# Optimization experiments

Hardware: AMD Instinct MI355X
Metric: run time of the kernel (lower is better)

## Reference

```python
import jax, jax.numpy as jnp
import numpy as np

NPOINT = 1024
RADIUS = 0.15
NSAMPLE = 32
BN_EPS = 1e-5


def farthest_point_sample(xyz, npoint):
    # xyz: [B, N, 3] -> idx [B, npoint]
    B, N, _ = xyz.shape

    def step(carry, _):
        dmin, far = carry
        cent = jnp.take_along_axis(xyz, far[:, None, None], axis=1)  # [B,1,3]
        d = jnp.sum((xyz - cent) ** 2, axis=-1)                      # [B,N]
        dmin = jnp.minimum(dmin, d)
        nxt = jnp.argmax(dmin, axis=-1).astype(jnp.int32)
        return (dmin, nxt), far

    init = (jnp.full((B, N), 1e10, xyz.dtype), jnp.zeros((B,), jnp.int32))
    _, idx = jax.lax.scan(step, init, None, length=npoint)
    return idx.T  # [B, npoint]


def ball_query(radius, nsample, xyz, new_xyz):
    # xyz: [B,N,3], new_xyz: [B,S,3] -> idx [B,S,nsample]
    B, S, _ = new_xyz.shape
    N = xyz.shape[1]
    sqr = jnp.sum((new_xyz[:, :, None, :] - xyz[:, None, :, :]) ** 2, axis=-1)  # [B,S,N]
    ar = jnp.broadcast_to(jnp.arange(N, dtype=jnp.int32), (B, S, N))
    gidx = jnp.where(sqr > radius * radius, N, ar)
    gidx = jnp.sort(gidx, axis=-1)[:, :, :nsample]
    first = gidx[:, :, :1]
    return jnp.where(gidx == N, first, gidx)


def setup_inputs() -> dict:
    key = jax.random.key(0)
    ks = jax.random.split(key, 8)
    B, N, Cin, Cmlp, Cout = 8, 4096, 64, 128, 256
    xyz = jax.random.uniform(ks[0], (B, N, 3), dtype=jnp.float32)
    t = jax.random.normal(ks[1], (B, 128), dtype=jnp.float32)
    points = jax.random.normal(ks[2], (B, N, Cin), dtype=jnp.float32)
    W1 = jax.random.normal(ks[3], (Cin, Cmlp), dtype=jnp.float32) / np.sqrt(Cin)
    b1 = jnp.zeros((Cmlp,), jnp.float32)
    Wc = jax.random.normal(ks[4], (Cmlp, Cout), dtype=jnp.float32) / np.sqrt(Cmlp)
    bc = jnp.zeros((Cout,), jnp.float32)
    gamma = jnp.ones((Cout,), jnp.float32)
    beta = jnp.zeros((Cout,), jnp.float32)
    return {"xyz": xyz, "t": t, "points": points, "W1": W1, "b1": b1,
            "Wc": Wc, "bc": bc, "gamma": gamma, "beta": beta}


def reference(xyz, t, points, W1, b1, Wc, bc, gamma, beta):
    # t (time embedding) is unused in the visible (truncated) forward body.
    B, N, _ = xyz.shape
    # 1) farthest point sampling -> centers
    fps_idx = farthest_point_sample(xyz, NPOINT)                     # [B,S]
    new_xyz = jnp.take_along_axis(xyz, fps_idx[:, :, None], axis=1)  # [B,S,3]
    # 2) radius ball-query grouping
    gidx = ball_query(RADIUS, NSAMPLE, xyz, new_xyz)                 # [B,S,ns]
    # 3) pointwise MLP on features, then group (gather)
    feats = points @ W1 + b1                                          # [B,N,Cmlp]
    grouped = jax.vmap(lambda f, i: f[i])(feats, gidx)                # [B,S,ns,Cmlp]
    # 4) GroupConv: 1x1 conv + BatchNorm(train stats) + ReLU
    h = jnp.einsum('bsnc,co->bsno', grouped, Wc) + bc                 # [B,S,ns,Cout]
    mean = jnp.mean(h, axis=(0, 1, 2))
    var = jnp.var(h, axis=(0, 1, 2))
    h = jax.nn.relu((h - mean) / jnp.sqrt(var + BN_EPS) * gamma + beta)
    # 5) max-pool over neighborhood
    new_points = jnp.max(h, axis=2)                                   # [B,S,Cout]
    return new_points
```

## Files before the change

kernel.cpp:

```cpp
#include <hip/hip_runtime.h>
#include <stdint.h>

#define BN 8
#define NPT 4096
#define NS 1024
#define KS 32
#define CIN 64
#define CMID 128
#define COUT 256
#define NGRP (BN*NS)
#define NBINS 512

typedef short bf16x8 __attribute__((ext_vector_type(8)));
typedef float f32x4 __attribute__((ext_vector_type(4)));
typedef unsigned long long u64;

__device__ __forceinline__ float bf2f(unsigned short u){
  union { unsigned int i; float f; } v; v.i = ((unsigned int)u) << 16; return v.f;
}
__device__ __forceinline__ unsigned short f2bf(float f){
  union { float f; unsigned int i; } v; v.f = f;
  unsigned int r = (v.i + 0x7fffu + ((v.i >> 16) & 1u)) >> 16;
  return (unsigned short)r;
}
__device__ __forceinline__ uint32_t pack2(float a, float b){
  return (uint32_t)f2bf(a) | ((uint32_t)f2bf(b) << 16);
}
__device__ __forceinline__ float ldf(const void* p, size_t i, bool isbf){
  return isbf ? bf2f(((const unsigned short*)p)[i]) : ((const float*)p)[i];
}
__device__ __forceinline__ bool detect_bf(const void* gamma){
  return ((const unsigned int*)gamma)[0] == 0x3F803F80u;
}
template<int CTRL>
__device__ __forceinline__ u64 dpp_rot_u64(u64 x){
  int lo = (int)(unsigned int)(x & 0xFFFFFFFFull);
  int hi = (int)(unsigned int)(x >> 32);
  int nlo = __builtin_amdgcn_update_dpp(0, lo, CTRL, 0xF, 0xF, true);
  int nhi = __builtin_amdgcn_update_dpp(0, hi, CTRL, 0xF, 0xF, true);
  return ((u64)(unsigned int)nhi << 32) | (unsigned int)nlo;
}
__device__ __forceinline__ u64 u64max(u64 a, u64 b){ return a > b ? a : b; }

__device__ __forceinline__ unsigned mcode(float x, float y, float z){
  int ix = (int)(x*16.f); ix = ix<0?0:(ix>15?15:ix);
  int iy = (int)(y*16.f); iy = iy<0?0:(iy>15?15:iy);
  int iz = (int)(z*8.f);  iz = iz<0?0:(iz>7?7:iz);
  return ((unsigned)(iy&1))      | ((unsigned)(ix&1)<<1) | ((unsigned)(iz&1)<<2)
       | ((unsigned)(iy&2)<<2)   | ((unsigned)(ix&2)<<3) | ((unsigned)(iz&2)<<4)
       | ((unsigned)(iy&4)<<4)   | ((unsigned)(ix&4)<<5) | ((unsigned)(iz&4)<<6)
       | ((unsigned)(iy&8)<<6)   | ((unsigned)(ix&8)<<7);
}

__global__ __launch_bounds__(512, 4)
void k_front(const void* __restrict__ xyz,
             const void* __restrict__ points,
             const void* __restrict__ W1,
             const void* __restrict__ Wc,
             const void* __restrict__ gamma,
             float* __restrict__ newxyz,
             unsigned short* __restrict__ featsb,
             unsigned short* __restrict__ wct,
             float* __restrict__ ps, float* __restrict__ pq, int bigws)
{
  int tid = threadIdx.x;
  int bid = blockIdx.x;
  bool isbf = detect_bf(gamma);
  __shared__ __align__(16) char smem[65536];
  __shared__ unsigned tsum[512];
  __shared__ u64 wk[2][8];

  if (bid < 8){
    float* ssx = (float*)smem;
    float* ssy = ssx + NPT;
    float* ssz = ssy + NPT;
    unsigned short* snl = (unsigned short*)(ssz + NPT);
    unsigned* hist = (unsigned*)(smem + 57344);
    size_t xb = (size_t)bid*NPT*3;
    int base = tid*8;
    for (int i=tid; i<2048; i+=512) hist[i]=0;
    __syncthreads();
    unsigned codes[8];
    #pragma unroll
    for (int k=0;k<8;k++){
      size_t p = xb + (size_t)(base+k)*3;
      unsigned c = mcode(ldf(xyz,p,isbf), ldf(xyz,p+1,isbf), ldf(xyz,p+2,isbf));
      codes[k]=c;
      atomicAdd(&hist[c],1u);
    }
    __syncthreads();
    unsigned l0=hist[tid*4],l1=hist[tid*4+1],l2=hist[tid*4+2],l3=hist[tid*4+3];
    unsigned s = l0+l1+l2+l3;
    tsum[tid]=s; __syncthreads();
    for (int off=1; off<512; off<<=1){
      unsigned v = (tid>=off)? tsum[tid-off]:0u; __syncthreads();
      tsum[tid]+=v; __syncthreads();
    }
    unsigned ex = tsum[tid]-s;
    hist[tid*4]=ex; hist[tid*4+1]=ex+l0; hist[tid*4+2]=ex+l0+l1; hist[tid*4+3]=ex+l0+l1+l2;
    __syncthreads();
    #pragma unroll
    for (int k=0;k<8;k++){
      size_t p = xb + (size_t)(base+k)*3;
      float x=ldf(xyz,p,isbf), y=ldf(xyz,p+1,isbf), z=ldf(xyz,p+2,isbf);
      unsigned pos = atomicAdd(&hist[codes[k]],1u);
      ssx[pos]=x; ssy[pos]=y; ssz[pos]=z; snl[pos]=(unsigned short)(4095-(base+k));
    }
    __syncthreads();
    float qx0,qx1,qx2,qx3,qx4,qx5,qx6,qx7;
    float qy0,qy1,qy2,qy3,qy4,qy5,qy6,qy7;
    float qz0,qz1,qz2,qz3,qz4,qz5,qz6,qz7;
    float dd0,dd1,dd2,dd3,dd4,dd5,dd6,dd7;
    unsigned lk0,lk1,lk2,lk3,lk4,lk5,lk6,lk7;
#define LOADS(k) { int p=base+k; qx##k=ssx[p]; qy##k=ssy[p]; qz##k=ssz[p]; dd##k=1e10f; \
  lk##k = ((unsigned)snl[p]<<12) | (unsigned)p; }
    LOADS(0) LOADS(1) LOADS(2) LOADS(3) LOADS(4) LOADS(5) LOADS(6) LOADS(7)
#undef LOADS
    float bxl = fminf(fminf(fminf(qx0,qx1),fminf(qx2,qx3)),fminf(fminf(qx4,qx5),fminf(qx6,qx7)));
    float bxh = fmaxf(fmaxf(fmaxf(qx0,qx1),fmaxf(qx2,qx3)),fmaxf(fmaxf(qx4,qx5),fmaxf(qx6,qx7)));
    float byl = fminf(fminf(fminf(qy0,qy1),fminf(qy2,qy3)),fminf(fminf(qy4,qy5),fminf(qy6,qy7)));
    float byh = fmaxf(fmaxf(fmaxf(qy0,qy1),fmaxf(qy2,qy3)),fmaxf(fmaxf(qy4,qy5),fmaxf(qy6,qy7)));
    float bzl = fminf(fminf(fminf(qz0,qz1),fminf(qz2,qz3)),fminf(fminf(qz4,qz5),fminf(qz6,qz7)));
    float bzh = fmaxf(fmaxf(fmaxf(qz0,qz1),fmaxf(qz2,qz3)),fmaxf(fmaxf(qz4,qz5),fmaxf(qz6,qz7)));
    #pragma unroll
    for (int off=1; off<64; off<<=1){
      bxl = fminf(bxl, __shfl_xor(bxl,off,64)); bxh = fmaxf(bxh, __shfl_xor(bxh,off,64));
      byl = fminf(byl, __shfl_xor(byl,off,64)); byh = fmaxf(byh, __shfl_xor(byh,off,64));
      bzl = fminf(bzl, __shfl_xor(bzl,off,64)); bzh = fmaxf(bzh, __shfl_xor(bzh,off,64));
    }
    float cx=ldf(xyz,xb,isbf), cy=ldf(xyz,xb+1,isbf), cz=ldf(xyz,xb+2,isbf);
    if (tid==0){ float* o = newxyz + (size_t)bid*NS*3; o[0]=cx; o[1]=cy; o[2]=cz; }
    int lane = tid & 63, wv = tid >> 6;
    u64 ckey = ((u64)__float_as_uint(1e10f) << 32);
    for (int it=1; it<NS; ++it){
      int par = it & 1;
      float ex2 = fmaxf(fmaxf(__fsub_rn(bxl,cx), __fsub_rn(cx,bxh)), 0.f);
      float ey2 = fmaxf(fmaxf(__fsub_rn(byl,cy), __fsub_rn(cy,byh)), 0.f);
      float ez2 = fmaxf(fmaxf(__fsub_rn(bzl,cz), __fsub_rn(cz,bzh)), 0.f);
      float lb2 = ex2*ex2 + ey2*ey2 + ez2*ez2;
      float wtmax = __uint_as_float((unsigned)(ckey >> 32));
      bool act = !(lb2*0.999f >= wtmax);
      if (__builtin_amdgcn_readfirstlane((int)act)){
#define FPS_STEP(k) { float dx=__fsub_rn(qx##k,cx), dy=__fsub_rn(qy##k,cy), dz=__fsub_rn(qz##k,cz); \
  float d=__fadd_rn(__fadd_rn(__fmul_rn(dx,dx),__fmul_rn(dy,dy)),__fmul_rn(dz,dz)); \
  dd##k=fminf(dd##k,d); }
        FPS_STEP(0) FPS_STEP(1) FPS_STEP(2) FPS_STEP(3)
        FPS_STEP(4) FPS_STEP(5) FPS_STEP(6) FPS_STEP(7)
#undef FPS_STEP
#define KEYK(k) ( ((u64)__float_as_uint(dd##k) << 32) | lk##k )
        u64 e0=u64max(KEYK(0),KEYK(1)), e2=u64max(KEYK(2),KEYK(3));
        u64 e4=u64max(KEYK(4),KEYK(5)), e6=u64max(KEYK(6),KEYK(7));
#undef KEYK
        e0=u64max(e0,e2); e4=u64max(e4,e6);
        u64 key=u64max(e0,e4);
        key = u64max(key, dpp_rot_u64<0x121>(key));
        key = u64max(key, dpp_rot_u64<0x122>(key));
        key = u64max(key, dpp_rot_u64<0x124>(key));
        key = u64max(key, dpp_rot_u64<0x128>(key));
        key = u64max(key, __shfl_xor(key, 16, 64));
        key = u64max(key, __shfl_xor(key, 32, 64));
        ckey = key;
      }
      if (lane == 0) wk[par][wv] = ckey;
      __syncthreads();
      const u64* w8 = wk[par];
      u64 k0 = u64max(u64max(u64max(w8[0],w8[1]), u64max(w8[2],w8[3])),
                      u64max(u64max(w8[4],w8[5]), u64max(w8[6],w8[7])));
      unsigned spos = (unsigned)(k0 & 0xFFFu);
      cx = ssx[spos]; cy = ssy[spos]; cz = ssz[spos];
      if (tid==0){ float* o = newxyz + ((size_t)bid*NS + it)*3; o[0]=cx; o[1]=cy; o[2]=cz; }
    }
  } else if (bid == 8){
    for (int i=tid; i<CMID*COUT; i+=512){
      int k = i >> 8, n = i & 255;
      unsigned short w = isbf ? ((const unsigned short*)Wc)[i] : f2bf(((const float*)Wc)[i]);
      wct[(size_t)n*CMID + k] = w;
    }
    if (!bigws){
      for (int i=tid; i<COUT*NBINS; i+=512){ ps[i]=0.f; pq[i]=0.f; }
    }
  } else {
    float* w1s = (float*)smem;
    float* pts = (float*)(smem + 32768);
    int rb = bid - 9;
    int r0g = rb*64;
    for (int i=tid; i<CIN*CMID; i+=512) w1s[i] = ldf(W1, i, isbf);
    for (int i=tid; i<64*CIN; i+=512)   pts[i] = ldf(points, (size_t)r0g*CIN + i, isbf);
    __syncthreads();
    int o0 = (tid & 15) * 8, r0 = (tid >> 4) * 2;
    float acc0[8]={0,0,0,0,0,0,0,0}, acc1[8]={0,0,0,0,0,0,0,0};
    for (int c=0;c<CIN;c++){
      float a0 = pts[r0*CIN + c], a1 = pts[(r0+1)*CIN + c];
      const float* wr = &w1s[c*CMID + o0];
      #pragma unroll
      for (int j=0;j<8;j++){ acc0[j] = fmaf(a0, wr[j], acc0[j]); acc1[j] = fmaf(a1, wr[j], acc1[j]); }
    }
    unsigned short* f0 = featsb + ((size_t)(r0g + r0))*CMID + o0;
    uint4 u;
    u.x=pack2(acc0[0],acc0[1]); u.y=pack2(acc0[2],acc0[3]); u.z=pack2(acc0[4],acc0[5]); u.w=pack2(acc0[6],acc0[7]);
    *(uint4*)f0 = u;
    u.x=pack2(acc1[0],acc1[1]); u.y=pack2(acc1[2],acc1[3]); u.z=pack2(acc1[4],acc1[5]); u.w=pack2(acc1[6],acc1[7]);
    *(uint4*)(f0 + CMID) = u;
  }
}

__global__ __launch_bounds__(256)
void k_ballq(const void* __restrict__ xyz,
             const void* __restrict__ gamma,
             const float* __restrict__ newxyz,
             int* __restrict__ gidx)
{
  __shared__ float sp[NPT*3];
  __shared__ int slots[4][KS];
  int tid = threadIdx.x;
  bool isbf = detect_bf(gamma);
  int cb = blockIdx.x * 64;
  int b = cb >> 10;
  size_t xb = (size_t)b*NPT*3;
  for (int i=tid; i<NPT*3; i+=256) sp[i] = ldf(xyz, xb + i, isbf);
  __syncthreads();
  int lane = tid & 63, wv = tid >> 6;
  const float rr = (float)(0.15*0.15);
  for (int j=0; j<16; ++j){
    int cid = cb + wv*16 + j;
    const float* cc = newxyz + (size_t)cid*3;
    float cx=cc[0], cy=cc[1], cz=cc[2];
    int cnt = 0;
    for (int ch=0; ch<64; ++ch){
      int p = ch*64 + lane;
      float dx=__fsub_rn(sp[p*3],cx), dy=__fsub_rn(sp[p*3+1],cy), dz=__fsub_rn(sp[p*3+2],cz);
      float d=__fadd_rn(__fadd_rn(__fmul_rn(dx,dx),__fmul_rn(dy,dy)),__fmul_rn(dz,dz));
      bool in = !(d > rr);
      u64 mk = __ballot(in);
      int pos = cnt + __popcll(mk & ((1ull<<lane) - 1ull));
      if (in && pos < KS) slots[wv][pos] = p;
      cnt += __popcll(mk);
      if (cnt >= KS) break;
    }
    int total = cnt < KS ? cnt : KS;
    if (lane < KS){
      int v = (lane < total) ? slots[wv][lane] : slots[wv][0];
      gidx[(size_t)cid*KS + lane] = v;
    }
  }
}

__global__ __launch_bounds__(256)
void k_group(const unsigned short* __restrict__ featsb,
             const unsigned short* __restrict__ wct,
             const int* __restrict__ gidx,
             float* __restrict__ ps, float* __restrict__ pq,
             float* __restrict__ hM, int bigws)
{
  int tid = threadIdx.x;
  int bs0 = blockIdx.x * 2;
  __shared__ unsigned short g[2][32][136];
  __shared__ int gi[2][KS];
  if (tid < 2*KS) gi[tid>>5][tid&31] = gidx[(size_t)bs0*KS + tid];
  __syncthreads();
  {
    int r = tid >> 3, sg = tid & 7;
    size_t fb = (size_t)(bs0>>10)*NPT;
    #pragma unroll
    for (int gg=0; gg<2; gg++){
      const unsigned short* src = featsb + (fb + gi[gg][r])*CMID + sg*16;
      uint4 v0 = *(const uint4*)src;
      uint4 v1 = *(const uint4*)(src + 8);
      *(uint4*)(&g[gg][r][sg*16])     = v0;
      *(uint4*)(&g[gg][r][sg*16 + 8]) = v1;
    }
  }
  __syncthreads();
  int lane = tid & 63, wv = tid >> 6;
  int m = lane & 15, quad = lane >> 4;
  f32x4 acc[2][2][4];
  #pragma unroll
  for (int gg=0; gg<2; gg++)
    #pragma unroll
    for (int a=0;a<2;a++)
      #pragma unroll
      for (int b2=0;b2<4;b2++) acc[gg][a][b2] = (f32x4){0.f,0.f,0.f,0.f};
  int n0 = wv * 64;
  #pragma unroll
  for (int k0=0; k0<CMID; k0+=32){
    bf16x8 a00 = *(const bf16x8*)(&g[0][m][k0 + quad*8]);
    bf16x8 a01 = *(const bf16x8*)(&g[0][16 + m][k0 + quad*8]);
    bf16x8 a10 = *(const bf16x8*)(&g[1][m][k0 + quad*8]);
    bf16x8 a11 = *(const bf16x8*)(&g[1][16 + m][k0 + quad*8]);
    #pragma unroll
    for (int nt=0; nt<4; nt++){
      int n = n0 + nt*16 + m;
      bf16x8 bb = *(const bf16x8*)(wct + (size_t)n*CMID + k0 + quad*8);
      acc[0][0][nt] = __builtin_amdgcn_mfma_f32_16x16x32_bf16(a00, bb, acc[0][0][nt], 0, 0, 0);
      acc[0][1][nt] = __builtin_amdgcn_mfma_f32_16x16x32_bf16(a01, bb, acc[0][1][nt], 0, 0, 0);
      acc[1][0][nt] = __builtin_amdgcn_mfma_f32_16x16x32_bf16(a10, bb, acc[1][0][nt], 0, 0, 0);
      acc[1][1][nt] = __builtin_amdgcn_mfma_f32_16x16x32_bf16(a11, bb, acc[1][1][nt], 0, 0, 0);
    }
  }
  #pragma unroll
  for (int gg=0; gg<2; gg++){
    int bs = bs0 + gg;
    #pragma unroll
    for (int nt=0; nt<4; nt++){
      float s=0.f, q=0.f, hx=-3.402823466e38f;
      #pragma unroll
      for (int mt=0; mt<2; mt++)
        #pragma unroll
        for (int rg=0; rg<4; rg++){ float h = acc[gg][mt][nt][rg]; s += h; q += h*h; hx = fmaxf(hx,h); }
      s += __shfl_xor(s,16,64); q += __shfl_xor(q,16,64); hx = fmaxf(hx, __shfl_xor(hx,16,64));
      s += __shfl_xor(s,32,64); q += __shfl_xor(q,32,64); hx = fmaxf(hx, __shfl_xor(hx,32,64));
      if (quad == 0){
        int o = n0 + nt*16 + m;
        if (bigws){
          ps[(size_t)o*NGRP + bs] = s;
          pq[(size_t)o*NGRP + bs] = q;
        } else {
          atomicAdd(&ps[(size_t)o*NBINS + (bs & (NBINS-1))], s);
          atomicAdd(&pq[(size_t)o*NBINS + (bs & (NBINS-1))], q);
        }
        hM[(size_t)bs*COUT + o] = hx;
      }
    }
  }
}

__global__ __launch_bounds__(256)
void k_bnprep(const float* __restrict__ ps, const float* __restrict__ pq,
              const void* __restrict__ gamma, const void* __restrict__ beta,
              float* __restrict__ av, float* __restrict__ cv, int nbins)
{
  int tid = threadIdx.x, o = blockIdx.x;
  bool isbf = detect_bf(gamma);
  float s=0.f, q=0.f;
  for (int i=tid; i<nbins; i+=256){ s += ps[(size_t)o*nbins + i]; q += pq[(size_t)o*nbins + i]; }
  #pragma unroll
  for (int off=1; off<64; off<<=1){ s += __shfl_xor(s,off,64); q += __shfl_xor(q,off,64); }
  __shared__ float ls[4], lq[4];
  int lane = tid & 63, wv = tid >> 6;
  if (lane == 0){ ls[wv]=s; lq[wv]=q; }
  __syncthreads();
  if (tid == 0){
    float S = ls[0]+ls[1]+ls[2]+ls[3], Q = lq[0]+lq[1]+lq[2]+lq[3];
    const float invM = 1.0f/262144.0f;
    float mean = S*invM;
    float var  = fmaxf(Q*invM - mean*mean, 0.f);
    float inv  = 1.0f/sqrtf(var + 1e-5f);
    float a = ldf(gamma,o,isbf)*inv;
    float c = ldf(beta,o,isbf) - mean*a;
    av[o]=a; cv[o]=c;
  }
}

__global__ __launch_bounds__(256)
void k_bnfinal(const float* __restrict__ hM,
               const float* __restrict__ av, const float* __restrict__ cv,
               const void* __restrict__ gamma, void* __restrict__ out)
{
  int idx = blockIdx.x*256 + threadIdx.x;
  int o = idx & 255;
  float v = fmaxf(hM[idx]*av[o] + cv[o], 0.f);
  if (detect_bf(gamma)) ((unsigned short*)out)[idx] = f2bf(v);
  else                  ((float*)out)[idx] = v;
}

extern "C" void kernel_launch(void* const* d_in, const int* in_sizes, int n_in,
                              void* d_out, int out_size, void* d_ws, size_t ws_size,
                              hipStream_t stream)
{
  const void* xyz    = d_in[0];
  const void* points = d_in[2];
  const void* W1     = d_in[3];
  const void* Wc     = d_in[5];
  const void* gamma  = d_in[7];
  const void* beta   = d_in[8];

  char* ws = (char*)d_ws;
  unsigned short* featsb = (unsigned short*)(ws + 0);
  unsigned short* wct    = (unsigned short*)(ws + 8388608);
  float* newxyz          = (float*)(ws + 8454144);
  int*   gidx            = (int*)(ws + 8552448);
  bool bigws = ws_size >= (size_t)34768896;
  float *ps, *pq, *hM, *av, *cv;
  if (bigws){
    ps = (float*)(ws + 9601024);
    pq = (float*)(ws + 17989632);
    hM = (float*)(ws + 26378240);
    av = (float*)(ws + 34766848);
    cv = (float*)(ws + 34767872);
  } else {
    hM = (float*)(ws + 9601024);
    ps = (float*)(ws + 17989632);
    pq = (float*)(ws + 18513920);
    av = (float*)(ws + 19038208);
    cv = (float*)(ws + 19039232);
  }

  hipLaunchKernelGGL(k_front,  dim3(521), dim3(512), 0, stream,
                     xyz, points, W1, Wc, gamma, newxyz, featsb, wct, ps, pq, (int)bigws);
  hipLaunchKernelGGL(k_ballq,  dim3(128), dim3(256), 0, stream, xyz, gamma, newxyz, gidx);
  hipLaunchKernelGGL(k_group,  dim3(4096), dim3(256), 0, stream,
                     featsb, wct, gidx, ps, pq, hM, (int)bigws);
  hipLaunchKernelGGL(k_bnprep, dim3(256),  dim3(256), 0, stream,
                     ps, pq, gamma, beta, av, cv, bigws ? NGRP : NBINS);
  hipLaunchKernelGGL(k_bnfinal,dim3(8192), dim3(256), 0, stream, hM, av, cv, gamma, d_out);
}
```

Measured before the change: 953.8 us.

## Split FPS wave work into four spatial quarters with per-quarter bbox culling

Each wave's 512 Morton-sorted points are split into four contiguous 128-point quarters, each with its own bounding box and cached max-min-distance. Per iteration, a ballot decides which quarters can be affected by the new centroid, so only those quarters update distances and run a wave reduction. The reduction now uses DPP row_bcast plus readlane instead of shuffles. Finer culling should skip more distance work, at the cost of up to four reductions per iteration when many quarters are active.

```diff
diff --git a/kernel.cpp b/kernel.cpp
--- a/kernel.cpp
+++ b/kernel.cpp
@@ -33,7 +33,7 @@
   return ((const unsigned int*)gamma)[0] == 0x3F803F80u;
 }
 template<int CTRL>
-__device__ __forceinline__ u64 dpp_rot_u64(u64 x){
+__device__ __forceinline__ u64 dpp_u64(u64 x){
   int lo = (int)(unsigned int)(x & 0xFFFFFFFFull);
   int hi = (int)(unsigned int)(x >> 32);
   int nlo = __builtin_amdgcn_update_dpp(0, lo, CTRL, 0xF, 0xF, true);
@@ -41,6 +41,20 @@
   return ((u64)(unsigned int)nhi << 32) | (unsigned int)nlo;
 }
 __device__ __forceinline__ u64 u64max(u64 a, u64 b){ return a > b ? a : b; }
+__device__ __forceinline__ u64 wave_max_u64(u64 k){
+  k = u64max(k, dpp_u64<0x121>(k));
+  k = u64max(k, dpp_u64<0x122>(k));
+  k = u64max(k, dpp_u64<0x124>(k));
+  k = u64max(k, dpp_u64<0x128>(k));
+  k = u64max(k, dpp_u64<0x142>(k));
+  k = u64max(k, dpp_u64<0x143>(k));
+  return k;
+}
+__device__ __forceinline__ u64 readlane63_u64(u64 k){
+  unsigned lo = (unsigned)__builtin_amdgcn_readlane((int)(unsigned)(k & 0xFFFFFFFFull), 63);
+  unsigned hi = (unsigned)__builtin_amdgcn_readlane((int)(unsigned)(k >> 32), 63);
+  return ((u64)hi << 32) | lo;
+}
 
 __device__ __forceinline__ unsigned mcode(float x, float y, float z){
   int ix = (int)(x*16.f); ix = ix<0?0:(ix>15?15:ix);
@@ -96,8 +110,8 @@
       unsigned v = (tid>=off)? tsum[tid-off]:0u; __syncthreads();
       tsum[tid]+=v; __syncthreads();
     }
-    unsigned ex = tsum[tid]-s;
-    hist[tid*4]=ex; hist[tid*4+1]=ex+l0; hist[tid*4+2]=ex+l0+l1; hist[tid*4+3]=ex+l0+l1+l2;
+    unsigned ex0 = tsum[tid]-s;
+    hist[tid*4]=ex0; hist[tid*4+1]=ex0+l0; hist[tid*4+2]=ex0+l0+l1; hist[tid*4+3]=ex0+l0+l1+l2;
     __syncthreads();
     #pragma unroll
     for (int k=0;k<8;k++){
@@ -107,61 +121,67 @@
       ssx[pos]=x; ssy[pos]=y; ssz[pos]=z; snl[pos]=(unsigned short)(4095-(base+k));
     }
     __syncthreads();
+    int lane = tid & 63, wv = tid >> 6;
     float qx0,qx1,qx2,qx3,qx4,qx5,qx6,qx7;
     float qy0,qy1,qy2,qy3,qy4,qy5,qy6,qy7;
     float qz0,qz1,qz2,qz3,qz4,qz5,qz6,qz7;
     float dd0,dd1,dd2,dd3,dd4,dd5,dd6,dd7;
     unsigned lk0,lk1,lk2,lk3,lk4,lk5,lk6,lk7;
-#define LOADS(k) { int p=base+k; qx##k=ssx[p]; qy##k=ssy[p]; qz##k=ssz[p]; dd##k=1e10f; \
+#define LOADS(k) { int p = (wv<<9) + (((k)>>1)<<7) + (lane<<1) + ((k)&1); \
+  qx##k=ssx[p]; qy##k=ssy[p]; qz##k=ssz[p]; dd##k=1e10f; \
   lk##k = ((unsigned)snl[p]<<12) | (unsigned)p; }
     LOADS(0) LOADS(1) LOADS(2) LOADS(3) LOADS(4) LOADS(5) LOADS(6) LOADS(7)
 #undef LOADS
-    float bxl = fminf(fminf(fminf(qx0,qx1),fminf(qx2,qx3)),fminf(fminf(qx4,qx5),fminf(qx6,qx7)));
-    float bxh = fmaxf(fmaxf(fmaxf(qx0,qx1),fmaxf(qx2,qx3)),fmaxf(fmaxf(qx4,qx5),fmaxf(qx6,qx7)));
-    float byl = fminf(fminf(fminf(qy0,qy1),fminf(qy2,qy3)),fminf(fminf(qy4,qy5),fminf(qy6,qy7)));
-    float byh = fmaxf(fmaxf(fmaxf(qy0,qy1),fmaxf(qy2,qy3)),fmaxf(fmaxf(qy4,qy5),fmaxf(qy6,qy7)));
-    float bzl = fminf(fminf(fminf(qz0,qz1),fminf(qz2,qz3)),fminf(fminf(qz4,qz5),fminf(qz6,qz7)));
-    float bzh = fmaxf(fmaxf(fmaxf(qz0,qz1),fmaxf(qz2,qz3)),fmaxf(fmaxf(qz4,qz5),fmaxf(qz6,qz7)));
-    #pragma unroll
-    for (int off=1; off<64; off<<=1){
-      bxl = fminf(bxl, __shfl_xor(bxl,off,64)); bxh = fmaxf(bxh, __shfl_xor(bxh,off,64));
-      byl = fminf(byl, __shfl_xor(byl,off,64)); byh = fmaxf(byh, __shfl_xor(byh,off,64));
-      bzl = fminf(bzl, __shfl_xor(bzl,off,64)); bzh = fmaxf(bzh, __shfl_xor(bzh,off,64));
-    }
+    float qbxl, qbxh, qbyl, qbyh, qbzl, qbzh;
+    {
+      float bxl[4],bxh[4],byl[4],byh[4],bzl[4],bzh[4];
+#define BBOX(q,a,b) { \
+      float xl=fminf(qx##a,qx##b), xh=fmaxf(qx##a,qx##b); \
+      float yl=fminf(qy##a,qy##b), yh=fmaxf(qy##a,qy##b); \
+      float zl=fminf(qz##a,qz##b), zh=fmaxf(qz##a,qz##b); \
+      for (int off=1; off<64; off<<=1){ \
+        xl=fminf(xl,__shfl_xor(xl,off,64)); xh=fmaxf(xh,__shfl_xor(xh,off,64)); \
+        yl=fminf(yl,__shfl_xor(yl,off,64)); yh=fmaxf(yh,__shfl_xor(yh,off,64)); \
+        zl=fminf(zl,__shfl_xor(zl,off,64)); zh=fmaxf(zh,__shfl_xor(zh,off,64)); } \
+      bxl[q]=xl; bxh[q]=xh; byl[q]=yl; byh[q]=yh; bzl[q]=zl; bzh[q]=zh; }
+      BBOX(0,0,1) BBOX(1,2,3) BBOX(2,4,5) BBOX(3,6,7)
+#undef BBOX
+      int lq = lane & 3;
+      qbxl = lq==0?bxl[0]:(lq==1?bxl[1]:(lq==2?bxl[2]:bxl[3]));
+      qbxh = lq==0?bxh[0]:(lq==1?bxh[1]:(lq==2?bxh[2]:bxh[3]));
+      qbyl = lq==0?byl[0]:(lq==1?byl[1]:(lq==2?byl[2]:byl[3]));
+      qbyh = lq==0?byh[0]:(lq==1?byh[1]:(lq==2?byh[2]:byh[3]));
+      qbzl = lq==0?bzl[0]:(lq==1?bzl[1]:(lq==2?bzl[2]:bzl[3]));
+      qbzh = lq==0?bzh[0]:(lq==1?bzh[1]:(lq==2?bzh[2]:bzh[3]));
+    }
+    float qd = 1e10f;
+    u64 qk0=0, qk1=0, qk2=0, qk3=0;
     float cx=ldf(xyz,xb,isbf), cy=ldf(xyz,xb+1,isbf), cz=ldf(xyz,xb+2,isbf);
     if (tid==0){ float* o = newxyz + (size_t)bid*NS*3; o[0]=cx; o[1]=cy; o[2]=cz; }
-    int lane = tid & 63, wv = tid >> 6;
-    u64 ckey = ((u64)__float_as_uint(1e10f) << 32);
     for (int it=1; it<NS; ++it){
       int par = it & 1;
-      float ex2 = fmaxf(fmaxf(__fsub_rn(bxl,cx), __fsub_rn(cx,bxh)), 0.f);
-      float ey2 = fmaxf(fmaxf(__fsub_rn(byl,cy), __fsub_rn(cy,byh)), 0.f);
-      float ez2 = fmaxf(fmaxf(__fsub_rn(bzl,cz), __fsub_rn(cz,bzh)), 0.f);
-      float lb2 = ex2*ex2 + ey2*ey2 + ez2*ez2;
-      float wtmax = __uint_as_float((unsigned)(ckey >> 32));
-      bool act = !(lb2*0.999f >= wtmax);
-      if (__builtin_amdgcn_readfirstlane((int)act)){
+      float ex = fmaxf(fmaxf(qbxl - cx, cx - qbxh), 0.f);
+      float ey = fmaxf(fmaxf(qbyl - cy, cy - qbyh), 0.f);
+      float ez = fmaxf(fmaxf(qbzl - cz, cz - qbzh), 0.f);
+      float lb2 = ex*ex + ey*ey + ez*ez;
+      unsigned amask = (unsigned)__ballot(lb2*0.999f < qd) & 0xFu;
 #define FPS_STEP(k) { float dx=__fsub_rn(qx##k,cx), dy=__fsub_rn(qy##k,cy), dz=__fsub_rn(qz##k,cz); \
   float d=__fadd_rn(__fadd_rn(__fmul_rn(dx,dx),__fmul_rn(dy,dy)),__fmul_rn(dz,dz)); \
   dd##k=fminf(dd##k,d); }
-        FPS_STEP(0) FPS_STEP(1) FPS_STEP(2) FPS_STEP(3)
-        FPS_STEP(4) FPS_STEP(5) FPS_STEP(6) FPS_STEP(7)
+#define KEYK(k) ( ((u64)__float_as_uint(dd##k) << 32) | lk##k )
+#define QUPD(q,a,b) if (amask & (1u<<q)){ \
+      FPS_STEP(a) FPS_STEP(b) \
+      u64 kk = u64max(KEYK(a), KEYK(b)); \
+      kk = wave_max_u64(kk); \
+      qk##q = readlane63_u64(kk); \
+      float nm = __uint_as_float((unsigned)(qk##q >> 32)); \
+      qd = ((lane&3)==q) ? nm : qd; }
+      QUPD(0,0,1) QUPD(1,2,3) QUPD(2,4,5) QUPD(3,6,7)
+#undef QUPD
+#undef KEYK
 #undef FPS_STEP
-#define KEYK(k) ( ((u64)__float_as_uint(dd##k) << 32) | lk##k )
-        u64 e0=u64max(KEYK(0),KEYK(1)), e2=u64max(KEYK(2),KEYK(3));
-        u64 e4=u64max(KEYK(4),KEYK(5)), e6=u64max(KEYK(6),KEYK(7));
-#undef KEYK
-        e0=u64max(e0,e2); e4=u64max(e4,e6);
-        u64 key=u64max(e0,e4);
-        key = u64max(key, dpp_rot_u64<0x121>(key));
-        key = u64max(key, dpp_rot_u64<0x122>(key));
-        key = u64max(key, dpp_rot_u64<0x124>(key));
-        key = u64max(key, dpp_rot_u64<0x128>(key));
-        key = u64max(key, __shfl_xor(key, 16, 64));
-        key = u64max(key, __shfl_xor(key, 32, 64));
-        ckey = key;
-      }
-      if (lane == 0) wk[par][wv] = ckey;
+      u64 wkey = u64max(u64max(qk0,qk1), u64max(qk2,qk3));
+      if (lane == 0) wk[par][wv] = wkey;
       __syncthreads();
       const u64* w8 = wk[par];
       u64 k0 = u64max(u64max(u64max(w8[0],w8[1]), u64max(w8[2],w8[3])),
```

Measured after the change: 1.209 ms. 1.27x slower.

## Shrink FPS block to 4 waves with 16 points per thread and DPP row reductions

Applied to the files above, without the earlier changes.

The farthest-point-sampling blocks now use 256 threads, each holding 16 points instead of 8. The per-step block barrier therefore spans 4 waves instead of 8, and the cross-wave combine reads 4 keys. The wave argmax reduction now uses DPP row_bcast patterns plus a readlane of lane 63 instead of two shuffles. Doing so means more serial ALU work per thread per step and higher register pressure. The grid and per-block work of the other block roles are rescaled to match.

```diff
diff --git a/kernel.cpp b/kernel.cpp
--- a/kernel.cpp
+++ b/kernel.cpp
@@ -33,7 +33,7 @@
   return ((const unsigned int*)gamma)[0] == 0x3F803F80u;
 }
 template<int CTRL>
-__device__ __forceinline__ u64 dpp_rot_u64(u64 x){
+__device__ __forceinline__ u64 dpp_u64(u64 x){
   int lo = (int)(unsigned int)(x & 0xFFFFFFFFull);
   int hi = (int)(unsigned int)(x >> 32);
   int nlo = __builtin_amdgcn_update_dpp(0, lo, CTRL, 0xF, 0xF, true);
@@ -41,6 +41,20 @@
   return ((u64)(unsigned int)nhi << 32) | (unsigned int)nlo;
 }
 __device__ __forceinline__ u64 u64max(u64 a, u64 b){ return a > b ? a : b; }
+__device__ __forceinline__ u64 wave_max_u64(u64 k){
+  k = u64max(k, dpp_u64<0x121>(k));
+  k = u64max(k, dpp_u64<0x122>(k));
+  k = u64max(k, dpp_u64<0x124>(k));
+  k = u64max(k, dpp_u64<0x128>(k));
+  k = u64max(k, dpp_u64<0x142>(k));
+  k = u64max(k, dpp_u64<0x143>(k));
+  return k;
+}
+__device__ __forceinline__ u64 readlane63_u64(u64 k){
+  unsigned lo = (unsigned)__builtin_amdgcn_readlane((int)(unsigned)(k & 0xFFFFFFFFull), 63);
+  unsigned hi = (unsigned)__builtin_amdgcn_readlane((int)(unsigned)(k >> 32), 63);
+  return ((u64)hi << 32) | lo;
+}
 
 __device__ __forceinline__ unsigned mcode(float x, float y, float z){
   int ix = (int)(x*16.f); ix = ix<0?0:(ix>15?15:ix);
@@ -52,7 +66,7 @@
        | ((unsigned)(iy&8)<<6)   | ((unsigned)(ix&8)<<7);
 }
 
-__global__ __launch_bounds__(512, 4)
+__global__ __launch_bounds__(256, 2)
 void k_front(const void* __restrict__ xyz,
              const void* __restrict__ points,
              const void* __restrict__ W1,
@@ -67,8 +81,8 @@
   int bid = blockIdx.x;
   bool isbf = detect_bf(gamma);
   __shared__ __align__(16) char smem[65536];
-  __shared__ unsigned tsum[512];
-  __shared__ u64 wk[2][8];
+  __shared__ unsigned tsum[256];
+  __shared__ u64 wk[2][4];
 
   if (bid < 8){
     float* ssx = (float*)smem;
@@ -77,60 +91,73 @@
     unsigned short* snl = (unsigned short*)(ssz + NPT);
     unsigned* hist = (unsigned*)(smem + 57344);
     size_t xb = (size_t)bid*NPT*3;
-    int base = tid*8;
-    for (int i=tid; i<2048; i+=512) hist[i]=0;
+    int base = tid*16;
+    for (int i=tid; i<2048; i+=256) hist[i]=0;
     __syncthreads();
-    unsigned codes[8];
-    #pragma unroll
-    for (int k=0;k<8;k++){
+    unsigned codes[16];
+    #pragma unroll
+    for (int k=0;k<16;k++){
       size_t p = xb + (size_t)(base+k)*3;
       unsigned c = mcode(ldf(xyz,p,isbf), ldf(xyz,p+1,isbf), ldf(xyz,p+2,isbf));
       codes[k]=c;
       atomicAdd(&hist[c],1u);
     }
     __syncthreads();
-    unsigned l0=hist[tid*4],l1=hist[tid*4+1],l2=hist[tid*4+2],l3=hist[tid*4+3];
-    unsigned s = l0+l1+l2+l3;
+    unsigned lcnt[8]; unsigned s=0;
+    #pragma unroll
+    for (int j=0;j<8;j++){ lcnt[j]=hist[tid*8+j]; s+=lcnt[j]; }
     tsum[tid]=s; __syncthreads();
-    for (int off=1; off<512; off<<=1){
+    for (int off=1; off<256; off<<=1){
       unsigned v = (tid>=off)? tsum[tid-off]:0u; __syncthreads();
       tsum[tid]+=v; __syncthreads();
     }
     unsigned ex = tsum[tid]-s;
-    hist[tid*4]=ex; hist[tid*4+1]=ex+l0; hist[tid*4+2]=ex+l0+l1; hist[tid*4+3]=ex+l0+l1+l2;
+    #pragma unroll
+    for (int j=0;j<8;j++){ hist[tid*8+j]=ex; ex+=lcnt[j]; }
     __syncthreads();
     #pragma unroll
-    for (int k=0;k<8;k++){
+    for (int k=0;k<16;k++){
       size_t p = xb + (size_t)(base+k)*3;
       float x=ldf(xyz,p,isbf), y=ldf(xyz,p+1,isbf), z=ldf(xyz,p+2,isbf);
       unsigned pos = atomicAdd(&hist[codes[k]],1u);
       ssx[pos]=x; ssy[pos]=y; ssz[pos]=z; snl[pos]=(unsigned short)(4095-(base+k));
     }
     __syncthreads();
-    float qx0,qx1,qx2,qx3,qx4,qx5,qx6,qx7;
-    float qy0,qy1,qy2,qy3,qy4,qy5,qy6,qy7;
-    float qz0,qz1,qz2,qz3,qz4,qz5,qz6,qz7;
-    float dd0,dd1,dd2,dd3,dd4,dd5,dd6,dd7;
-    unsigned lk0,lk1,lk2,lk3,lk4,lk5,lk6,lk7;
-#define LOADS(k) { int p=base+k; qx##k=ssx[p]; qy##k=ssy[p]; qz##k=ssz[p]; dd##k=1e10f; \
+    int lane = tid & 63, wv = tid >> 6;
+    float qx0,qx1,qx2,qx3,qx4,qx5,qx6,qx7,qx8,qx9,qx10,qx11,qx12,qx13,qx14,qx15;
+    float qy0,qy1,qy2,qy3,qy4,qy5,qy6,qy7,qy8,qy9,qy10,qy11,qy12,qy13,qy14,qy15;
+    float qz0,qz1,qz2,qz3,qz4,qz5,qz6,qz7,qz8,qz9,qz10,qz11,qz12,qz13,qz14,qz15;
+    float dd0,dd1,dd2,dd3,dd4,dd5,dd6,dd7,dd8,dd9,dd10,dd11,dd12,dd13,dd14,dd15;
+    unsigned lk0,lk1,lk2,lk3,lk4,lk5,lk6,lk7,lk8,lk9,lk10,lk11,lk12,lk13,lk14,lk15;
+#define LOADS(k) { int p = base+(k); qx##k=ssx[p]; qy##k=ssy[p]; qz##k=ssz[p]; dd##k=1e10f; \
   lk##k = ((unsigned)snl[p]<<12) | (unsigned)p; }
     LOADS(0) LOADS(1) LOADS(2) LOADS(3) LOADS(4) LOADS(5) LOADS(6) LOADS(7)
+    LOADS(8) LOADS(9) LOADS(10) LOADS(11) LOADS(12) LOADS(13) LOADS(14) LOADS(15)
 #undef LOADS
-    float bxl = fminf(fminf(fminf(qx0,qx1),fminf(qx2,qx3)),fminf(fminf(qx4,qx5),fminf(qx6,qx7)));
-    float bxh = fmaxf(fmaxf(fmaxf(qx0,qx1),fmaxf(qx2,qx3)),fmaxf(fmaxf(qx4,qx5),fmaxf(qx6,qx7)));
-    float byl = fminf(fminf(fminf(qy0,qy1),fminf(qy2,qy3)),fminf(fminf(qy4,qy5),fminf(qy6,qy7)));
-    float byh = fmaxf(fmaxf(fmaxf(qy0,qy1),fmaxf(qy2,qy3)),fmaxf(fmaxf(qy4,qy5),fmaxf(qy6,qy7)));
-    float bzl = fminf(fminf(fminf(qz0,qz1),fminf(qz2,qz3)),fminf(fminf(qz4,qz5),fminf(qz6,qz7)));
-    float bzh = fmaxf(fmaxf(fmaxf(qz0,qz1),fmaxf(qz2,qz3)),fmaxf(fmaxf(qz4,qz5),fmaxf(qz6,qz7)));
-    #pragma unroll
-    for (int off=1; off<64; off<<=1){
-      bxl = fminf(bxl, __shfl_xor(bxl,off,64)); bxh = fmaxf(bxh, __shfl_xor(bxh,off,64));
-      byl = fminf(byl, __shfl_xor(byl,off,64)); byh = fmaxf(byh, __shfl_xor(byh,off,64));
-      bzl = fminf(bzl, __shfl_xor(bzl,off,64)); bzh = fmaxf(bzh, __shfl_xor(bzh,off,64));
+    float bxl,bxh,byl,byh,bzl,bzh;
+    {
+      float xl = fminf(fminf(fminf(fminf(qx0,qx1),fminf(qx2,qx3)),fminf(fminf(qx4,qx5),fminf(qx6,qx7))),
+                       fminf(fminf(fminf(qx8,qx9),fminf(qx10,qx11)),fminf(fminf(qx12,qx13),fminf(qx14,qx15))));
+      float xh = fmaxf(fmaxf(fmaxf(fmaxf(qx0,qx1),fmaxf(qx2,qx3)),fmaxf(fmaxf(qx4,qx5),fmaxf(qx6,qx7))),
+                       fmaxf(fmaxf(fmaxf(qx8,qx9),fmaxf(qx10,qx11)),fmaxf(fmaxf(qx12,qx13),fmaxf(qx14,qx15))));
+      float yl = fminf(fminf(fminf(fminf(qy0,qy1),fminf(qy2,qy3)),fminf(fminf(qy4,qy5),fminf(qy6,qy7))),
+                       fminf(fminf(fminf(qy8,qy9),fminf(qy10,qy11)),fminf(fminf(qy12,qy13),fminf(qy14,qy15))));
+      float yh = fmaxf(fmaxf(fmaxf(fmaxf(qy0,qy1),fmaxf(qy2,qy3)),fmaxf(fmaxf(qy4,qy5),fmaxf(qy6,qy7))),
+                       fmaxf(fmaxf(fmaxf(qy8,qy9),fmaxf(qy10,qy11)),fmaxf(fmaxf(qy12,qy13),fmaxf(qy14,qy15))));
+      float zl = fminf(fminf(fminf(fminf(qz0,qz1),fminf(qz2,qz3)),fminf(fminf(qz4,qz5),fminf(qz6,qz7))),
+                       fminf(fminf(fminf(qz8,qz9),fminf(qz10,qz11)),fminf(fminf(qz12,qz13),fminf(qz14,qz15))));
+      float zh = fmaxf(fmaxf(fmaxf(fmaxf(qz0,qz1),fmaxf(qz2,qz3)),fmaxf(fmaxf(qz4,qz5),fmaxf(qz6,qz7))),
+                       fmaxf(fmaxf(fmaxf(qz8,qz9),fmaxf(qz10,qz11)),fmaxf(fmaxf(qz12,qz13),fmaxf(qz14,qz15))));
+      #pragma unroll
+      for (int off=1; off<64; off<<=1){
+        xl=fminf(xl,__shfl_xor(xl,off,64)); xh=fmaxf(xh,__shfl_xor(xh,off,64));
+        yl=fminf(yl,__shfl_xor(yl,off,64)); yh=fmaxf(yh,__shfl_xor(yh,off,64));
+        zl=fminf(zl,__shfl_xor(zl,off,64)); zh=fmaxf(zh,__shfl_xor(zh,off,64));
+      }
+      bxl=xl; bxh=xh; byl=yl; byh=yh; bzl=zl; bzh=zh;
     }
     float cx=ldf(xyz,xb,isbf), cy=ldf(xyz,xb+1,isbf), cz=ldf(xyz,xb+2,isbf);
     if (tid==0){ float* o = newxyz + (size_t)bid*NS*3; o[0]=cx; o[1]=cy; o[2]=cz; }
-    int lane = tid & 63, wv = tid >> 6;
     u64 ckey = ((u64)__float_as_uint(1e10f) << 32);
     for (int it=1; it<NS; ++it){
       int par = it & 1;
@@ -146,46 +173,44 @@
   dd##k=fminf(dd##k,d); }
         FPS_STEP(0) FPS_STEP(1) FPS_STEP(2) FPS_STEP(3)
         FPS_STEP(4) FPS_STEP(5) FPS_STEP(6) FPS_STEP(7)
+        FPS_STEP(8) FPS_STEP(9) FPS_STEP(10) FPS_STEP(11)
+        FPS_STEP(12) FPS_STEP(13) FPS_STEP(14) FPS_STEP(15)
 #undef FPS_STEP
 #define KEYK(k) ( ((u64)__float_as_uint(dd##k) << 32) | lk##k )
-        u64 e0=u64max(KEYK(0),KEYK(1)), e2=u64max(KEYK(2),KEYK(3));
-        u64 e4=u64max(KEYK(4),KEYK(5)), e6=u64max(KEYK(6),KEYK(7));
+        u64 t0=u64max(KEYK(0),KEYK(1)),  t1=u64max(KEYK(2),KEYK(3));
+        u64 t2=u64max(KEYK(4),KEYK(5)),  t3=u64max(KEYK(6),KEYK(7));
+        u64 t4=u64max(KEYK(8),KEYK(9)),  t5=u64max(KEYK(10),KEYK(11));
+        u64 t6=u64max(KEYK(12),KEYK(13)),t7=u64max(KEYK(14),KEYK(15));
 #undef KEYK
-        e0=u64max(e0,e2); e4=u64max(e4,e6);
-        u64 key=u64max(e0,e4);
-        key = u64max(key, dpp_rot_u64<0x121>(key));
-        key = u64max(key, dpp_rot_u64<0x122>(key));
-        key = u64max(key, dpp_rot_u64<0x124>(key));
-        key = u64max(key, dpp_rot_u64<0x128>(key));
-        key = u64max(key, __shfl_xor(key, 16, 64));
-        key = u64max(key, __shfl_xor(key, 32, 64));
-        ckey = key;
+        t0=u64max(t0,t1); t2=u64max(t2,t3); t4=u64max(t4,t5); t6=u64max(t6,t7);
+        t0=u64max(t0,t2); t4=u64max(t4,t6);
+        u64 key = u64max(t0,t4);
+        ckey = readlane63_u64(wave_max_u64(key));
       }
       if (lane == 0) wk[par][wv] = ckey;
       __syncthreads();
-      const u64* w8 = wk[par];
-      u64 k0 = u64max(u64max(u64max(w8[0],w8[1]), u64max(w8[2],w8[3])),
-                      u64max(u64max(w8[4],w8[5]), u64max(w8[6],w8[7])));
+      u64 k0 = u64max(u64max(wk[par][0], wk[par][1]),
+                      u64max(wk[par][2], wk[par][3]));
       unsigned spos = (unsigned)(k0 & 0xFFFu);
       cx = ssx[spos]; cy = ssy[spos]; cz = ssz[spos];
       if (tid==0){ float* o = newxyz + ((size_t)bid*NS + it)*3; o[0]=cx; o[1]=cy; o[2]=cz; }
     }
   } else if (bid == 8){
-    for (int i=tid; i<CMID*COUT; i+=512){
+    for (int i=tid; i<CMID*COUT; i+=256){
       int k = i >> 8, n = i & 255;
       unsigned short w = isbf ? ((const unsigned short*)Wc)[i] : f2bf(((const float*)Wc)[i]);
       wct[(size_t)n*CMID + k] = w;
     }
     if (!bigws){
-      for (int i=tid; i<COUT*NBINS; i+=512){ ps[i]=0.f; pq[i]=0.f; }
+      for (int i=tid; i<COUT*NBINS; i+=256){ ps[i]=0.f; pq[i]=0.f; }
     }
   } else {
     float* w1s = (float*)smem;
     float* pts = (float*)(smem + 32768);
     int rb = bid - 9;
-    int r0g = rb*64;
-    for (int i=tid; i<CIN*CMID; i+=512) w1s[i] = ldf(W1, i, isbf);
-    for (int i=tid; i<64*CIN; i+=512)   pts[i] = ldf(points, (size_t)r0g*CIN + i, isbf);
+    int r0g = rb*32;
+    for (int i=tid; i<CIN*CMID; i+=256) w1s[i] = ldf(W1, i, isbf);
+    for (int i=tid; i<32*CIN; i+=256)   pts[i] = ldf(points, (size_t)r0g*CIN + i, isbf);
     __syncthreads();
     int o0 = (tid & 15) * 8, r0 = (tid >> 4) * 2;
     float acc0[8]={0,0,0,0,0,0,0,0}, acc1[8]={0,0,0,0,0,0,0,0};
@@ -395,7 +420,7 @@
     cv = (float*)(ws + 19039232);
   }
 
-  hipLaunchKernelGGL(k_front,  dim3(521), dim3(512), 0, stream,
+  hipLaunchKernelGGL(k_front,  dim3(1033), dim3(256), 0, stream,
                      xyz, points, W1, Wc, gamma, newxyz, featsb, wct, ps, pq, (int)bigws);
   hipLaunchKernelGGL(k_ballq,  dim3(128), dim3(256), 0, stream, xyz, gamma, newxyz, gidx);
   hipLaunchKernelGGL(k_group,  dim3(4096), dim3(256), 0, stream,
```

Result: slower. 1.022 ms (+7.1%).
